# Performance work log

Hardware: AMD Instinct MI355X
Metric: run time of the kernel (lower is better)

Reference implementation:

```python
import jax, jax.numpy as jnp
import numpy as np

B, N, D, S = 16, 128, 128, 128   # batch, n_nodes, node/edge feat dim, state_dim
MP_INT = 256
UP_INT = 256
EPS = 1e-3  # keras BatchNormalization default epsilon


def _mlp(x, W1, b1, W2, b2):
    # Dense(relu) -> Dense(relu)
    h = jax.nn.relu(x @ W1 + b1)
    return jax.nn.relu(h @ W2 + b2)


def setup_inputs() -> dict:
    key = jax.random.key(0)
    ks = jax.random.split(key, 16)
    g = lambda k, shape: jax.random.normal(k, shape, dtype=jnp.float32) * 0.05
    nodes = jax.random.normal(ks[0], (B, N, D), dtype=jnp.float32)
    edges = jax.random.normal(ks[1], (B, N * N, D), dtype=jnp.float32)
    mask = (jax.random.uniform(ks[2], (B, N * N, 1)) > 0.5).astype(jnp.float32)
    return {
        "nodes": nodes, "edges": edges, "mask": mask,
        # Adj_Updater_1: concat(node_i, node_j, edge_ij) -> UP_INT -> S
        "W1a": g(ks[3], (3 * D, UP_INT)), "b1a": jnp.zeros((UP_INT,), jnp.float32),
        "W2a": g(ks[4], (UP_INT, S)), "b2a": jnp.zeros((S,), jnp.float32),
        # Message_Passer_1: concat(node_i, node_j, new_edge) -> MP_INT -> S
        "W1m": g(ks[5], (2 * D + S, MP_INT)), "b1m": jnp.zeros((MP_INT,), jnp.float32),
        "W2m": g(ks[6], (MP_INT, S)), "b2m": jnp.zeros((S,), jnp.float32),
        # Update_Func_1: concat(old_state, agg_messages) -> UP_INT -> S
        "W1u": g(ks[7], (D + S, UP_INT)), "b1u": jnp.zeros((UP_INT,), jnp.float32),
        "W2u": g(ks[8], (UP_INT, S)), "b2u": jnp.zeros((S,), jnp.float32),
        # BatchNorm (inference mode: moving stats) for nodes and edges
        "gamma_n": jnp.ones((S,), jnp.float32), "beta_n": jnp.zeros((S,), jnp.float32),
        "mean_n": jnp.zeros((S,), jnp.float32), "var_n": jnp.ones((S,), jnp.float32),
        "gamma_e": jnp.ones((S,), jnp.float32), "beta_e": jnp.zeros((S,), jnp.float32),
        "mean_e": jnp.zeros((S,), jnp.float32), "var_e": jnp.ones((S,), jnp.float32),
    }


def reference(nodes, edges, mask,
              W1a, b1a, W2a, b2a,
              W1m, b1m, W2m, b2m,
              W1u, b1u, W2u, b2u,
              gamma_n, beta_n, mean_n, var_n,
              gamma_e, beta_e, mean_e, var_e):
    b, n, d = nodes.shape
    # tf.tile(nodes,[1,n,1]): row p*n+q -> nodes[q]  (state_i)
    state_i = jnp.broadcast_to(nodes[:, None, :, :], (b, n, n, d)).reshape(b, n * n, d)
    # reshape(tile(nodes,[1,1,n])): row p*n+q -> nodes[p]  (state_j)
    state_j = jnp.broadcast_to(nodes[:, :, None, :], (b, n, n, d)).reshape(b, n * n, d)

    new_edges = _mlp(jnp.concatenate([state_i, state_j, edges], axis=-1), W1a, b1a, W2a, b2a)
    new_edges = new_edges * mask

    messages = _mlp(jnp.concatenate([state_i, state_j, new_edges], axis=-1), W1m, b1m, W2m, b2m)
    masked = (messages * mask).reshape(b, n, n, -1)
    agg_m = masked.sum(axis=2)  # reduce over axis 2 as in Message_Agg

    state_1 = _mlp(jnp.concatenate([nodes, agg_m], axis=-1), W1u, b1u, W2u, b2u)

    bn = lambda x, g_, b_, m_, v_: g_ * (x - m_) * jax.lax.rsqrt(v_ + EPS) + b_
    nodes_out = bn(state_1, gamma_n, beta_n, mean_n, var_n)
    edges_out = bn(new_edges, gamma_e, beta_e, mean_e, var_e)
    return nodes_out, edges_out
```

## Files before the change

### kernel.cpp

```cpp
#include <hip/hip_runtime.h>
#include <hip/hip_bf16.h>
#include <cstdint>
#include <cstddef>


typedef __attribute__((ext_vector_type(8))) __bf16 bf16x8;
typedef __attribute__((ext_vector_type(4))) float f32x4;

#define GLDS(gp, lp)                                                        \
  __builtin_amdgcn_global_load_lds(                                         \
      (const __attribute__((address_space(1))) void*)(gp),                  \
      (__attribute__((address_space(3))) void*)(lp), 16, 0, 0)

__device__ inline bf16x8 load8_cvt(const float* __restrict__ p) {
  const float4 a = *(const float4*)p;
  const float4 b = *(const float4*)(p + 4);
  bf16x8 r;
  r[0] = (__bf16)a.x; r[1] = (__bf16)a.y; r[2] = (__bf16)a.z; r[3] = (__bf16)a.w;
  r[4] = (__bf16)b.x; r[5] = (__bf16)b.y; r[6] = (__bf16)b.z; r[7] = (__bf16)b.w;
  return r;
}

__global__ void __launch_bounds__(256) proj_kernel(
    const float* __restrict__ nodes, const float* __restrict__ W1a,
    const float* __restrict__ b1a, const float* __restrict__ W1m,
    const float* __restrict__ b1m, const float* __restrict__ ge,
    const float* __restrict__ be, const float* __restrict__ me,
    const float* __restrict__ ve, float* __restrict__ outP,
    float* __restrict__ agg) {
  __shared__ float x[8][128];
  const int mat = blockIdx.y;
  const int t = threadIdx.x;
  if (mat == 0) {
#pragma unroll
    for (int i = 0; i < 4; ++i) agg[blockIdx.x * 1024 + i * 256 + t] = 0.f;
  }
  const float* W = (mat < 2 ? W1a : W1m) + ((mat & 1) ? 128 * 256 : 0);
  float* out = outP + (size_t)mat * (2048 * 256);
  const int r0 = blockIdx.x * 8;
  for (int i = t; i < 1024; i += 256)
    x[i >> 7][i & 127] = nodes[r0 * 128 + i];
  __syncthreads();
  float bv = 0.f;
  if (mat == 1) bv = b1a[t];
  if (mat == 3) {
    bv = b1m[t];
    const float* We = W1m + 65536;
    float cc = 0.f;
    for (int k = 0; k < 128; ++k) {
      float sc = ge[k] * rsqrtf(ve[k] + 1e-3f);
      float sh = be[k] - me[k] * sc;
      cc -= (sh / sc) * We[k * 256 + t];
    }
    bv += cc;
  }
  float acc[8];
#pragma unroll
  for (int r = 0; r < 8; ++r) acc[r] = bv;
  for (int k = 0; k < 128; ++k) {
    float w = W[k * 256 + t];
#pragma unroll
    for (int r = 0; r < 8; ++r) acc[r] += x[r][k] * w;
  }
  if (mat == 0 || mat == 2) {
    const int bb = r0 >> 7, q0 = r0 & 127;
    float* o = out + ((size_t)((bb << 8) + t) << 7) + q0;
#pragma unroll
    for (int r = 0; r < 8; ++r) o[r] = acc[r];
  } else {
    for (int r = 0; r < 8; ++r) out[(size_t)(r0 + r) * 256 + t] = acc[r];
  }
}

__global__ void __launch_bounds__(256) wswz_kernel(
    const float* __restrict__ W1a, const float* __restrict__ W2a,
    const float* __restrict__ W1m, const float* __restrict__ W2m,
    const float* __restrict__ ge, const float* __restrict__ ve,
    __hip_bfloat16* __restrict__ dstp) {
  __bf16* dst = (__bf16*)dstp;
  const int mat = blockIdx.y;
  const float* src;
  __bf16* d;
  int nsh;
  if (mat == 0)      { src = W1a + 65536; d = dst;         nsh = 8; }
  else if (mat == 1) { src = W2a;         d = dst + 32768; nsh = 7; }
  else if (mat == 2) { src = W1m + 65536; d = dst + 65536; nsh = 8; }
  else               { src = W2m;         d = dst + 98304; nsh = 7; }
  const int nmask = (1 << nsh) - 1;
  const int base = (blockIdx.x * 256 + threadIdx.x) * 4;
#pragma unroll
  for (int i = 0; i < 4; ++i) {
    int s = base + i;
    int k = s >> nsh, n = s & nmask;
    float v = src[s];
    if (mat == 2) v *= sqrtf(ve[k] + 1e-3f) / ge[k];
    int g = k >> 3;
    if (nsh == 8) {
      int gs = (g & 8) | ((g ^ n) & 7);
      d[n * 128 + gs * 8 + (k & 7)] = (__bf16)v;
    } else {
      int gs = (g ^ n) & 7;
      d[((k >> 6) << 13) + (n << 6) + (gs << 3) + (k & 7)] = (__bf16)v;
    }
  }
}

__global__ void __launch_bounds__(512, 2) edge_mlp_kernel(
    const float* __restrict__ edges, const float* __restrict__ mask,
    const float* __restrict__ b2a, const float* __restrict__ ge,
    const float* __restrict__ be, const float* __restrict__ me,
    const float* __restrict__ ve, const float* __restrict__ PaT,
    const float* __restrict__ Qab, const __hip_bfloat16* __restrict__ Wsw,
    float* __restrict__ edges_out) {
  __shared__ __align__(16) char sW[131072];
  __shared__ __align__(16) char sH1[16384];

  const int t = threadIdx.x;
  const int lane = t & 63, wv = t >> 6;
  const int cl = lane & 15, qd = lane >> 4;
  const int m0 = wv << 4;

  {
    const char* g = (const char*)Wsw;
    for (int o = wv * 1024; o < 131072; o += 8192)
      GLDS(g + o + lane * 16, sW + o);
  }
  float b2v[8], scv[8], shv[8];
#pragma unroll
  for (int nt = 0; nt < 8; ++nt) {
    const int col = nt * 16 + cl;
    b2v[nt] = b2a[col];
    float sc = ge[col] * rsqrtf(ve[col] + 1e-3f);
    scv[nt] = sc;
    shv[nt] = be[col] - me[col] * sc;
  }
  __syncthreads();

  const int tile0 = blockIdx.x * 8;
  const int bb = tile0 >> 7;

  bf16x8 xfA[4];
  {
    const float* Xb = edges + ((size_t)tile0 << 14);
#pragma unroll
    for (int ks = 0; ks < 4; ++ks)
      xfA[ks] = load8_cvt(Xb + (m0 + cl) * 128 + ks * 32 + qd * 8);
  }

#pragma unroll 1
  for (int ti = 0; ti < 8; ++ti) {
    const int p = (tile0 + ti) & 127;
    bf16x8 xfN[4];
    {
      const float* Xb = edges + ((size_t)(tile0 + ((ti + 1) & 7)) << 14);
#pragma unroll
      for (int ks = 0; ks < 4; ++ks)
        xfN[ks] = load8_cvt(Xb + (m0 + cl) * 128 + ks * 32 + qd * 8);
    }
    const float4 mv =
        *(const float4*)&mask[(bb << 14) + (p << 7) + m0 + qd * 4];
    const float* Qr = Qab + ((size_t)((bb << 7) + p) << 8);

    f32x4 ne[8];
#pragma unroll
    for (int nt = 0; nt < 8; ++nt)
      ne[nt] = (f32x4){b2v[nt], b2v[nt], b2v[nt], b2v[nt]};

#pragma unroll
    for (int h = 0; h < 4; ++h) {
      f32x4 a1[4];
#pragma unroll
      for (int nt = 0; nt < 4; ++nt) {
        const int col = h * 64 + nt * 16 + cl;
        const float qv = Qr[col];
        const float4 pa =
            *(const float4*)&PaT[((size_t)((bb << 8) + col) << 7) + m0 + qd * 4];
        a1[nt] = (f32x4){pa.x + qv, pa.y + qv, pa.z + qv, pa.w + qv};
      }
#pragma unroll
      for (int ks = 0; ks < 4; ++ks)
#pragma unroll
        for (int nt = 0; nt < 4; ++nt) {
          const int nl = nt * 16 + cl;
          const int g = ks * 4 + qd;
          const int gs = (g & 8) | ((g ^ nl) & 7);
          bf16x8 bw = *(const bf16x8*)(sW + (h * 64 + nl) * 256 + gs * 16);
          a1[nt] = __builtin_amdgcn_mfma_f32_16x16x32_bf16(xfA[ks], bw, a1[nt], 0, 0, 0);
        }
#pragma unroll
      for (int nt = 0; nt < 4; ++nt) {
        const int kq = nt * 16 + cl;
#pragma unroll
        for (int r = 0; r < 4; ++r) {
          const int m = m0 + qd * 4 + r;
          float v = a1[nt][r];
          v = v > 0.f ? v : 0.f;
          *(__bf16*)(sH1 + m * 128 + ((((kq >> 3) ^ m) & 7) << 4) +
                     ((kq & 7) << 1)) = (__bf16)v;
        }
      }
      bf16x8 hf[2];
#pragma unroll
      for (int ks = 0; ks < 2; ++ks) {
        const int m = m0 + cl;
        const int gs = ((ks * 4 + qd) ^ m) & 7;
        hf[ks] = *(const bf16x8*)(sH1 + m * 128 + gs * 16);
      }
#pragma unroll
      for (int ks = 0; ks < 2; ++ks)
#pragma unroll
        for (int nt = 0; nt < 8; ++nt) {
          const int n = nt * 16 + cl;
          const int gs = ((ks * 4 + qd) ^ n) & 7;
          bf16x8 bw =
              *(const bf16x8*)(sW + 65536 + h * 16384 + n * 128 + gs * 16);
          ne[nt] = __builtin_amdgcn_mfma_f32_16x16x32_bf16(hf[ks], bw, ne[nt], 0, 0, 0);
        }
    }
    float* Ob = edges_out + ((size_t)(tile0 + ti) << 14);
#pragma unroll
    for (int nt = 0; nt < 8; ++nt) {
      const int col = nt * 16 + cl;
#pragma unroll
      for (int r = 0; r < 4; ++r) {
        const int m = m0 + qd * 4 + r;
        float v = ne[nt][r];
        v = v > 0.f ? v : 0.f;
        const float mr = (r == 0 ? mv.x : r == 1 ? mv.y : r == 2 ? mv.z : mv.w);
        Ob[m * 128 + col] = (v * mr) * scv[nt] + shv[nt];
      }
    }
#pragma unroll
    for (int i = 0; i < 4; ++i) xfA[i] = xfN[i];
  }
}

__global__ void __launch_bounds__(512, 2) msg_mlp_kernel(
    const float* __restrict__ Yedges, const float* __restrict__ mask,
    const float* __restrict__ b2m, const float* __restrict__ PmT,
    const float* __restrict__ Qmb, const __hip_bfloat16* __restrict__ Wsw,
    float* __restrict__ agg) {
  __shared__ __align__(16) char sW[131072];
  __shared__ __align__(16) char sH1[16384];

  const int t = threadIdx.x;
  const int lane = t & 63, wv = t >> 6;
  const int cl = lane & 15, qd = lane >> 4;
  const int m0 = wv << 4;

  {
    const char* g = (const char*)Wsw;
    for (int o = wv * 1024; o < 131072; o += 8192)
      GLDS(g + o + lane * 16, sW + o);
  }
  float b2v[8];
#pragma unroll
  for (int nt = 0; nt < 8; ++nt) b2v[nt] = b2m[nt * 16 + cl];
  __syncthreads();

  const int tile0 = blockIdx.x * 8;
  const int bb = tile0 >> 7;

  bf16x8 xfA[4];
  {
    const float* Xb = Yedges + ((size_t)tile0 << 14);
#pragma unroll
    for (int ks = 0; ks < 4; ++ks)
      xfA[ks] = load8_cvt(Xb + (m0 + cl) * 128 + ks * 32 + qd * 8);
  }

#pragma unroll 1
  for (int ti = 0; ti < 8; ++ti) {
    const int p = (tile0 + ti) & 127;
    bf16x8 xfN[4];
    {
      const float* Xb = Yedges + ((size_t)(tile0 + ((ti + 1) & 7)) << 14);
#pragma unroll
      for (int ks = 0; ks < 4; ++ks)
        xfN[ks] = load8_cvt(Xb + (m0 + cl) * 128 + ks * 32 + qd * 8);
    }
    const float4 mv =
        *(const float4*)&mask[(bb << 14) + (p << 7) + m0 + qd * 4];
    const float* Qr = Qmb + ((size_t)((bb << 7) + p) << 8);

    f32x4 ms[8];
#pragma unroll
    for (int nt = 0; nt < 8; ++nt)
      ms[nt] = (f32x4){b2v[nt], b2v[nt], b2v[nt], b2v[nt]};

#pragma unroll
    for (int h = 0; h < 4; ++h) {
      f32x4 a1[4];
#pragma unroll
      for (int nt = 0; nt < 4; ++nt) {
        const int col = h * 64 + nt * 16 + cl;
        const float qv = Qr[col];
        const float4 pa =
            *(const float4*)&PmT[((size_t)((bb << 8) + col) << 7) + m0 + qd * 4];
        a1[nt] = (f32x4){pa.x + qv, pa.y + qv, pa.z + qv, pa.w + qv};
      }
#pragma unroll
      for (int ks = 0; ks < 4; ++ks)
#pragma unroll
        for (int nt = 0; nt < 4; ++nt) {
          const int nl = nt * 16 + cl;
          const int g = ks * 4 + qd;
          const int gs = (g & 8) | ((g ^ nl) & 7);
          bf16x8 bw = *(const bf16x8*)(sW + (h * 64 + nl) * 256 + gs * 16);
          a1[nt] = __builtin_amdgcn_mfma_f32_16x16x32_bf16(xfA[ks], bw, a1[nt], 0, 0, 0);
        }
#pragma unroll
      for (int nt = 0; nt < 4; ++nt) {
        const int kq = nt * 16 + cl;
#pragma unroll
        for (int r = 0; r < 4; ++r) {
          const int m = m0 + qd * 4 + r;
          float v = a1[nt][r];
          v = v > 0.f ? v : 0.f;
          *(__bf16*)(sH1 + m * 128 + ((((kq >> 3) ^ m) & 7) << 4) +
                     ((kq & 7) << 1)) = (__bf16)v;
        }
      }
      bf16x8 hf[2];
#pragma unroll
      for (int ks = 0; ks < 2; ++ks) {
        const int m = m0 + cl;
        const int gs = ((ks * 4 + qd) ^ m) & 7;
        hf[ks] = *(const bf16x8*)(sH1 + m * 128 + gs * 16);
      }
#pragma unroll
      for (int ks = 0; ks < 2; ++ks)
#pragma unroll
        for (int nt = 0; nt < 8; ++nt) {
          const int n = nt * 16 + cl;
          const int gs = ((ks * 4 + qd) ^ n) & 7;
          bf16x8 bw =
              *(const bf16x8*)(sW + 65536 + h * 16384 + n * 128 + gs * 16);
          ms[nt] = __builtin_amdgcn_mfma_f32_16x16x32_bf16(hf[ks], bw, ms[nt], 0, 0, 0);
        }
    }
#pragma unroll
    for (int nt = 0; nt < 8; ++nt) {
      float s = 0.f;
#pragma unroll
      for (int r = 0; r < 4; ++r) {
        float v = ms[nt][r];
        v = v > 0.f ? v : 0.f;
        const float mr = (r == 0 ? mv.x : r == 1 ? mv.y : r == 2 ? mv.z : mv.w);
        s += v * mr;
      }
      s += __shfl_xor(s, 16);
      s += __shfl_xor(s, 32);
      if (lane < 16)
        atomicAdd(&agg[((size_t)((bb << 7) + p) << 7) + nt * 16 + lane], s);
    }
#pragma unroll
    for (int i = 0; i < 4; ++i) xfA[i] = xfN[i];
  }
}

__global__ void __launch_bounds__(256) update_kernel(
    const float* __restrict__ nodes, const float* __restrict__ agg,
    const float* __restrict__ W1u, const float* __restrict__ b1u,
    const float* __restrict__ W2u, const float* __restrict__ b2u,
    const float* __restrict__ gn, const float* __restrict__ btn,
    const float* __restrict__ mn, const float* __restrict__ vn,
    float* __restrict__ out) {
  __shared__ float x[8][256];
  __shared__ float hh[8][256];
  const int t = threadIdx.x;
  const int r0 = blockIdx.x * 8;
  for (int i = t; i < 2048; i += 256) {
    int r = i >> 8, c = i & 255;
    x[r][c] = (c < 128) ? nodes[(r0 + r) * 128 + c] : agg[(r0 + r) * 128 + (c - 128)];
  }
  __syncthreads();
  float acc[8];
  {
    float bv = b1u[t];
#pragma unroll
    for (int r = 0; r < 8; ++r) acc[r] = bv;
  }
  for (int k = 0; k < 256; ++k) {
    float w = W1u[k * 256 + t];
#pragma unroll
    for (int r = 0; r < 8; ++r) acc[r] += x[r][k] * w;
  }
#pragma unroll
  for (int r = 0; r < 8; ++r) hh[r][t] = acc[r] > 0.f ? acc[r] : 0.f;
  __syncthreads();
  const int j = t & 127, half = t >> 7;
  float a2[4];
  {
    float bv = b2u[j];
#pragma unroll
    for (int r = 0; r < 4; ++r) a2[r] = bv;
  }
  for (int k = 0; k < 256; ++k) {
    float w = W2u[k * 128 + j];
#pragma unroll
    for (int r = 0; r < 4; ++r) a2[r] += hh[half * 4 + r][k] * w;
  }
  float sc = gn[j] * rsqrtf(vn[j] + 1e-3f);
  float sh = btn[j] - mn[j] * sc;
#pragma unroll
  for (int r = 0; r < 4; ++r) {
    float v = a2[r] > 0.f ? a2[r] : 0.f;
    out[(r0 + half * 4 + r) * 128 + j] = v * sc + sh;
  }
}

extern "C" void kernel_launch(void* const* d_in, const int* in_sizes, int n_in,
                              void* d_out, int out_size, void* d_ws,
                              size_t ws_size, hipStream_t stream) {
  (void)in_sizes; (void)n_in; (void)out_size; (void)ws_size;
  const float* nodes = (const float*)d_in[0];
  const float* edges = (const float*)d_in[1];
  const float* mask = (const float*)d_in[2];
  const float* W1a = (const float*)d_in[3];
  const float* b1a = (const float*)d_in[4];
  const float* W2a = (const float*)d_in[5];
  const float* b2a = (const float*)d_in[6];
  const float* W1m = (const float*)d_in[7];
  const float* b1m = (const float*)d_in[8];
  const float* W2m = (const float*)d_in[9];
  const float* b2m = (const float*)d_in[10];
  const float* W1u = (const float*)d_in[11];
  const float* b1u = (const float*)d_in[12];
  const float* W2u = (const float*)d_in[13];
  const float* b2u = (const float*)d_in[14];
  const float* gn = (const float*)d_in[15];
  const float* btn = (const float*)d_in[16];
  const float* mn = (const float*)d_in[17];
  const float* vn = (const float*)d_in[18];
  const float* ge = (const float*)d_in[19];
  const float* be = (const float*)d_in[20];
  const float* me = (const float*)d_in[21];
  const float* ve = (const float*)d_in[22];

  float* out_nodes = (float*)d_out;
  float* out_edges = (float*)d_out + 262144;

  char* ws = (char*)d_ws;
  float* PaT = (float*)(ws);
  float* Qab = (float*)(ws + ((size_t)1 << 21));
  float* PmT = (float*)(ws + ((size_t)2 << 21));
  float* Qmb = (float*)(ws + ((size_t)3 << 21));
  float* agg = (float*)(ws + ((size_t)4 << 21));
  __hip_bfloat16* Wsw = (__hip_bfloat16*)(ws + ((size_t)4 << 21) + ((size_t)1 << 20));

  proj_kernel<<<dim3(256, 4), 256, 0, stream>>>(nodes, W1a, b1a, W1m, b1m, ge,
                                                be, me, ve, PaT, agg);
  wswz_kernel<<<dim3(32, 4), 256, 0, stream>>>(W1a, W2a, W1m, W2m, ge, ve, Wsw);
  edge_mlp_kernel<<<256, 512, 0, stream>>>(edges, mask, b2a, ge, be, me, ve,
                                           PaT, Qab, Wsw, out_edges);
  msg_mlp_kernel<<<256, 512, 0, stream>>>(out_edges, mask, b2m, PmT, Qmb,
                                          Wsw + 65536, agg);
  update_kernel<<<256, 256, 0, stream>>>(nodes, agg, W1u, b1u, W2u, b2u, gn, btn,
                                         mn, vn, out_nodes);
}
```

Before: 524.4 us.

## Give each wave two 16-row M tiles and process two p-tiles per pass

In the edge and message MLP kernels, each wave now computes two 16-row M subtiles. Each B fragment read from shared memory therefore feeds two MFMAs, which halves LDS weight traffic per output. The 8 waves are split into two groups that handle two different p tiles at once, so each block runs 4 passes instead of 8. Each wave gets a private H1 scratch area in shared memory. Block indices are also swizzled to change which blocks run at the same time, and the next tile's input prefetch moves to after the first layer-1 chunk. The cost is more accumulator registers per wave (2x8 f32x4 plus 2x4 for layer 1), which may cause spills or lower occupancy under launch_bounds(512,2).

```diff
diff --git a/kernel.cpp b/kernel.cpp
--- a/kernel.cpp
+++ b/kernel.cpp
@@ -118,7 +118,9 @@
   const int t = threadIdx.x;
   const int lane = t & 63, wv = t >> 6;
   const int cl = lane & 15, qd = lane >> 4;
-  const int m0 = wv << 4;
+  const int tsel = wv >> 2;
+  const int wrow = (wv & 3) * 32;
+  char* const sH1w = sH1 + wv * 2048;
 
   {
     const char* g = (const char*)Wsw;
@@ -136,47 +138,56 @@
   }
   __syncthreads();
 
-  const int tile0 = blockIdx.x * 8;
-  const int bb = tile0 >> 7;
-
-  bf16x8 xfA[4];
+  const int bid = blockIdx.x;
+  const int sw = ((bid & 7) << 5) + (bid >> 3);
+  const int bb = sw >> 4;
+  const int pbase = (sw & 15) * 8;
+  const float* PaTb = PaT + ((size_t)bb << 15);
+
+  bf16x8 xf[2][4], xfN[2][4];
   {
-    const float* Xb = edges + ((size_t)tile0 << 14);
-#pragma unroll
-    for (int ks = 0; ks < 4; ++ks)
-      xfA[ks] = load8_cvt(Xb + (m0 + cl) * 128 + ks * 32 + qd * 8);
+    const float* Xb = edges + ((size_t)((bb << 7) + pbase + tsel) << 14);
+#pragma unroll
+    for (int mt = 0; mt < 2; ++mt)
+#pragma unroll
+      for (int ks = 0; ks < 4; ++ks)
+        xf[mt][ks] = load8_cvt(Xb + (wrow + mt * 16 + cl) * 128 + ks * 32 + qd * 8);
   }
 
 #pragma unroll 1
-  for (int ti = 0; ti < 8; ++ti) {
-    const int p = (tile0 + ti) & 127;
-    bf16x8 xfN[4];
-    {
-      const float* Xb = edges + ((size_t)(tile0 + ((ti + 1) & 7)) << 14);
-#pragma unroll
-      for (int ks = 0; ks < 4; ++ks)
-        xfN[ks] = load8_cvt(Xb + (m0 + cl) * 128 + ks * 32 + qd * 8);
-    }
-    const float4 mv =
-        *(const float4*)&mask[(bb << 14) + (p << 7) + m0 + qd * 4];
+  for (int pass = 0; pass < 4; ++pass) {
+    const int p = pbase + pass * 2 + tsel;
     const float* Qr = Qab + ((size_t)((bb << 7) + p) << 8);
-
-    f32x4 ne[8];
-#pragma unroll
-    for (int nt = 0; nt < 8; ++nt)
-      ne[nt] = (f32x4){b2v[nt], b2v[nt], b2v[nt], b2v[nt]};
+    float qv[4][4];
+#pragma unroll
+    for (int h = 0; h < 4; ++h)
+#pragma unroll
+      for (int nt = 0; nt < 4; ++nt) qv[h][nt] = Qr[h * 64 + nt * 16 + cl];
+    float4 mv[2];
+#pragma unroll
+    for (int mt = 0; mt < 2; ++mt)
+      mv[mt] = *(const float4*)&mask[(bb << 14) + (p << 7) + wrow + mt * 16 + qd * 4];
+
+    f32x4 ne[2][8];
+#pragma unroll
+    for (int mt = 0; mt < 2; ++mt)
+#pragma unroll
+      for (int nt = 0; nt < 8; ++nt)
+        ne[mt][nt] = (f32x4){b2v[nt], b2v[nt], b2v[nt], b2v[nt]};
 
 #pragma unroll
     for (int h = 0; h < 4; ++h) {
-      f32x4 a1[4];
-#pragma unroll
-      for (int nt = 0; nt < 4; ++nt) {
-        const int col = h * 64 + nt * 16 + cl;
-        const float qv = Qr[col];
-        const float4 pa =
-            *(const float4*)&PaT[((size_t)((bb << 8) + col) << 7) + m0 + qd * 4];
-        a1[nt] = (f32x4){pa.x + qv, pa.y + qv, pa.z + qv, pa.w + qv};
-      }
+      f32x4 a1[2][4];
+#pragma unroll
+      for (int mt = 0; mt < 2; ++mt)
+#pragma unroll
+        for (int nt = 0; nt < 4; ++nt) {
+          const int col = h * 64 + nt * 16 + cl;
+          const float4 pa =
+              *(const float4*)&PaTb[((size_t)col << 7) + wrow + mt * 16 + qd * 4];
+          const float q = qv[h][nt];
+          a1[mt][nt] = (f32x4){pa.x + q, pa.y + q, pa.z + q, pa.w + q};
+        }
 #pragma unroll
       for (int ks = 0; ks < 4; ++ks)
 #pragma unroll
@@ -185,26 +196,38 @@
           const int g = ks * 4 + qd;
           const int gs = (g & 8) | ((g ^ nl) & 7);
           bf16x8 bw = *(const bf16x8*)(sW + (h * 64 + nl) * 256 + gs * 16);
-          a1[nt] = __builtin_amdgcn_mfma_f32_16x16x32_bf16(xfA[ks], bw, a1[nt], 0, 0, 0);
-        }
-#pragma unroll
-      for (int nt = 0; nt < 4; ++nt) {
-        const int kq = nt * 16 + cl;
-#pragma unroll
-        for (int r = 0; r < 4; ++r) {
-          const int m = m0 + qd * 4 + r;
-          float v = a1[nt][r];
-          v = v > 0.f ? v : 0.f;
-          *(__bf16*)(sH1 + m * 128 + ((((kq >> 3) ^ m) & 7) << 4) +
-                     ((kq & 7) << 1)) = (__bf16)v;
-        }
+          a1[0][nt] = __builtin_amdgcn_mfma_f32_16x16x32_bf16(xf[0][ks], bw, a1[0][nt], 0, 0, 0);
+          a1[1][nt] = __builtin_amdgcn_mfma_f32_16x16x32_bf16(xf[1][ks], bw, a1[1][nt], 0, 0, 0);
+        }
+      if (h == 0 && pass < 3) {
+        const float* Xb = edges + ((size_t)((bb << 7) + p + 2) << 14);
+#pragma unroll
+        for (int mt = 0; mt < 2; ++mt)
+#pragma unroll
+          for (int ks = 0; ks < 4; ++ks)
+            xfN[mt][ks] =
+                load8_cvt(Xb + (wrow + mt * 16 + cl) * 128 + ks * 32 + qd * 8);
       }
-      bf16x8 hf[2];
-#pragma unroll
-      for (int ks = 0; ks < 2; ++ks) {
-        const int m = m0 + cl;
-        const int gs = ((ks * 4 + qd) ^ m) & 7;
-        hf[ks] = *(const bf16x8*)(sH1 + m * 128 + gs * 16);
+      bf16x8 hf[2][2];
+#pragma unroll
+      for (int mt = 0; mt < 2; ++mt) {
+#pragma unroll
+        for (int nt = 0; nt < 4; ++nt) {
+          const int kq = nt * 16 + cl;
+#pragma unroll
+          for (int r = 0; r < 4; ++r) {
+            const int m = qd * 4 + r;
+            float v = a1[mt][nt][r];
+            v = v > 0.f ? v : 0.f;
+            *(__bf16*)(sH1w + m * 128 + ((((kq >> 3) ^ m) & 7) << 4) +
+                       ((kq & 7) << 1)) = (__bf16)v;
+          }
+        }
+#pragma unroll
+        for (int ks = 0; ks < 2; ++ks) {
+          const int gs = ((ks * 4 + qd) ^ cl) & 7;
+          hf[mt][ks] = *(const bf16x8*)(sH1w + cl * 128 + gs * 16);
+        }
       }
 #pragma unroll
       for (int ks = 0; ks < 2; ++ks)
@@ -214,24 +237,32 @@
           const int gs = ((ks * 4 + qd) ^ n) & 7;
           bf16x8 bw =
               *(const bf16x8*)(sW + 65536 + h * 16384 + n * 128 + gs * 16);
-          ne[nt] = __builtin_amdgcn_mfma_f32_16x16x32_bf16(hf[ks], bw, ne[nt], 0, 0, 0);
-        }
-    }
-    float* Ob = edges_out + ((size_t)(tile0 + ti) << 14);
-#pragma unroll
-    for (int nt = 0; nt < 8; ++nt) {
-      const int col = nt * 16 + cl;
-#pragma unroll
-      for (int r = 0; r < 4; ++r) {
-        const int m = m0 + qd * 4 + r;
-        float v = ne[nt][r];
-        v = v > 0.f ? v : 0.f;
-        const float mr = (r == 0 ? mv.x : r == 1 ? mv.y : r == 2 ? mv.z : mv.w);
-        Ob[m * 128 + col] = (v * mr) * scv[nt] + shv[nt];
+          ne[0][nt] = __builtin_amdgcn_mfma_f32_16x16x32_bf16(hf[0][ks], bw, ne[0][nt], 0, 0, 0);
+          ne[1][nt] = __builtin_amdgcn_mfma_f32_16x16x32_bf16(hf[1][ks], bw, ne[1][nt], 0, 0, 0);
+        }
+    }
+    float* Ob = edges_out + ((size_t)((bb << 7) + p) << 14);
+#pragma unroll
+    for (int mt = 0; mt < 2; ++mt)
+#pragma unroll
+      for (int nt = 0; nt < 8; ++nt) {
+        const int col = nt * 16 + cl;
+#pragma unroll
+        for (int r = 0; r < 4; ++r) {
+          const int m = wrow + mt * 16 + qd * 4 + r;
+          float v = ne[mt][nt][r];
+          v = v > 0.f ? v : 0.f;
+          const float mr =
+              (r == 0 ? mv[mt].x : r == 1 ? mv[mt].y : r == 2 ? mv[mt].z : mv[mt].w);
+          Ob[m * 128 + col] = (v * mr) * scv[nt] + shv[nt];
+        }
       }
-    }
-#pragma unroll
-    for (int i = 0; i < 4; ++i) xfA[i] = xfN[i];
+    if (pass < 3) {
+#pragma unroll
+      for (int mt = 0; mt < 2; ++mt)
+#pragma unroll
+        for (int ks = 0; ks < 4; ++ks) xf[mt][ks] = xfN[mt][ks];
+    }
   }
 }
 
@@ -246,7 +277,9 @@
   const int t = threadIdx.x;
   const int lane = t & 63, wv = t >> 6;
   const int cl = lane & 15, qd = lane >> 4;
-  const int m0 = wv << 4;
+  const int tsel = wv >> 2;
+  const int wrow = (wv & 3) * 32;
+  char* const sH1w = sH1 + wv * 2048;
 
   {
     const char* g = (const char*)Wsw;
@@ -258,47 +291,56 @@
   for (int nt = 0; nt < 8; ++nt) b2v[nt] = b2m[nt * 16 + cl];
   __syncthreads();
 
-  const int tile0 = blockIdx.x * 8;
-  const int bb = tile0 >> 7;
-
-  bf16x8 xfA[4];
+  const int bid = blockIdx.x;
+  const int sw = ((bid & 7) << 5) + (bid >> 3);
+  const int bb = sw >> 4;
+  const int pbase = (sw & 15) * 8;
+  const float* PmTb = PmT + ((size_t)bb << 15);
+
+  bf16x8 xf[2][4], xfN[2][4];
   {
-    const float* Xb = Yedges + ((size_t)tile0 << 14);
-#pragma unroll
-    for (int ks = 0; ks < 4; ++ks)
-      xfA[ks] = load8_cvt(Xb + (m0 + cl) * 128 + ks * 32 + qd * 8);
+    const float* Xb = Yedges + ((size_t)((bb << 7) + pbase + tsel) << 14);
+#pragma unroll
+    for (int mt = 0; mt < 2; ++mt)
+#pragma unroll
+      for (int ks = 0; ks < 4; ++ks)
+        xf[mt][ks] = load8_cvt(Xb + (wrow + mt * 16 + cl) * 128 + ks * 32 + qd * 8);
   }
 
 #pragma unroll 1
-  for (int ti = 0; ti < 8; ++ti) {
-    const int p = (tile0 + ti) & 127;
-    bf16x8 xfN[4];
-    {
-      const float* Xb = Yedges + ((size_t)(tile0 + ((ti + 1) & 7)) << 14);
-#pragma unroll
-      for (int ks = 0; ks < 4; ++ks)
-        xfN[ks] = load8_cvt(Xb + (m0 + cl) * 128 + ks * 32 + qd * 8);
-    }
-    const float4 mv =
-        *(const float4*)&mask[(bb << 14) + (p << 7) + m0 + qd * 4];
+  for (int pass = 0; pass < 4; ++pass) {
+    const int p = pbase + pass * 2 + tsel;
     const float* Qr = Qmb + ((size_t)((bb << 7) + p) << 8);
-
-    f32x4 ms[8];
-#pragma unroll
-    for (int nt = 0; nt < 8; ++nt)
-      ms[nt] = (f32x4){b2v[nt], b2v[nt], b2v[nt], b2v[nt]};
+    float qv[4][4];
+#pragma unroll
+    for (int h = 0; h < 4; ++h)
+#pragma unroll
+      for (int nt = 0; nt < 4; ++nt) qv[h][nt] = Qr[h * 64 + nt * 16 + cl];
+    float4 mv[2];
+#pragma unroll
+    for (int mt = 0; mt < 2; ++mt)
+      mv[mt] = *(const float4*)&mask[(bb << 14) + (p << 7) + wrow + mt * 16 + qd * 4];
+
+    f32x4 ms[2][8];
+#pragma unroll
+    for (int mt = 0; mt < 2; ++mt)
+#pragma unroll
+      for (int nt = 0; nt < 8; ++nt)
+        ms[mt][nt] = (f32x4){b2v[nt], b2v[nt], b2v[nt], b2v[nt]};
 
 #pragma unroll
     for (int h = 0; h < 4; ++h) {
-      f32x4 a1[4];
-#pragma unroll
-      for (int nt = 0; nt < 4; ++nt) {
-        const int col = h * 64 + nt * 16 + cl;
-        const float qv = Qr[col];
-        const float4 pa =
-            *(const float4*)&PmT[((size_t)((bb << 8) + col) << 7) + m0 + qd * 4];
-        a1[nt] = (f32x4){pa.x + qv, pa.y + qv, pa.z + qv, pa.w + qv};
-      }
+      f32x4 a1[2][4];
+#pragma unroll
+      for (int mt = 0; mt < 2; ++mt)
+#pragma unroll
+        for (int nt = 0; nt < 4; ++nt) {
+          const int col = h * 64 + nt * 16 + cl;
+          const float4 pa =
+              *(const float4*)&PmTb[((size_t)col << 7) + wrow + mt * 16 + qd * 4];
+          const float q = qv[h][nt];
+          a1[mt][nt] = (f32x4){pa.x + q, pa.y + q, pa.z + q, pa.w + q};
+        }
 #pragma unroll
       for (int ks = 0; ks < 4; ++ks)
 #pragma unroll
@@ -307,26 +349,38 @@
           const int g = ks * 4 + qd;
           const int gs = (g & 8) | ((g ^ nl) & 7);
           bf16x8 bw = *(const bf16x8*)(sW + (h * 64 + nl) * 256 + gs * 16);
-          a1[nt] = __builtin_amdgcn_mfma_f32_16x16x32_bf16(xfA[ks], bw, a1[nt], 0, 0, 0);
-        }
-#pragma unroll
-      for (int nt = 0; nt < 4; ++nt) {
-        const int kq = nt * 16 + cl;
-#pragma unroll
-        for (int r = 0; r < 4; ++r) {
-          const int m = m0 + qd * 4 + r;
-          float v = a1[nt][r];
-          v = v > 0.f ? v : 0.f;
-          *(__bf16*)(sH1 + m * 128 + ((((kq >> 3) ^ m) & 7) << 4) +
-                     ((kq & 7) << 1)) = (__bf16)v;
-        }
+          a1[0][nt] = __builtin_amdgcn_mfma_f32_16x16x32_bf16(xf[0][ks], bw, a1[0][nt], 0, 0, 0);
+          a1[1][nt] = __builtin_amdgcn_mfma_f32_16x16x32_bf16(xf[1][ks], bw, a1[1][nt], 0, 0, 0);
+        }
+      if (h == 0 && pass < 3) {
+        const float* Xb = Yedges + ((size_t)((bb << 7) + p + 2) << 14);
+#pragma unroll
+        for (int mt = 0; mt < 2; ++mt)
+#pragma unroll
+          for (int ks = 0; ks < 4; ++ks)
+            xfN[mt][ks] =
+                load8_cvt(Xb + (wrow + mt * 16 + cl) * 128 + ks * 32 + qd * 8);
       }
-      bf16x8 hf[2];
-#pragma unroll
-      for (int ks = 0; ks < 2; ++ks) {
-        const int m = m0 + cl;
-        const int gs = ((ks * 4 + qd) ^ m) & 7;
-        hf[ks] = *(const bf16x8*)(sH1 + m * 128 + gs * 16);
+      bf16x8 hf[2][2];
+#pragma unroll
+      for (int mt = 0; mt < 2; ++mt) {
+#pragma unroll
+        for (int nt = 0; nt < 4; ++nt) {
+          const int kq = nt * 16 + cl;
+#pragma unroll
+          for (int r = 0; r < 4; ++r) {
+            const int m = qd * 4 + r;
+            float v = a1[mt][nt][r];
+            v = v > 0.f ? v : 0.f;
+            *(__bf16*)(sH1w + m * 128 + ((((kq >> 3) ^ m) & 7) << 4) +
+                       ((kq & 7) << 1)) = (__bf16)v;
+          }
+        }
+#pragma unroll
+        for (int ks = 0; ks < 2; ++ks) {
+          const int gs = ((ks * 4 + qd) ^ cl) & 7;
+          hf[mt][ks] = *(const bf16x8*)(sH1w + cl * 128 + gs * 16);
+        }
       }
 #pragma unroll
       for (int ks = 0; ks < 2; ++ks)
@@ -336,26 +390,34 @@
           const int gs = ((ks * 4 + qd) ^ n) & 7;
           bf16x8 bw =
               *(const bf16x8*)(sW + 65536 + h * 16384 + n * 128 + gs * 16);
-          ms[nt] = __builtin_amdgcn_mfma_f32_16x16x32_bf16(hf[ks], bw, ms[nt], 0, 0, 0);
+          ms[0][nt] = __builtin_amdgcn_mfma_f32_16x16x32_bf16(hf[0][ks], bw, ms[0][nt], 0, 0, 0);
+          ms[1][nt] = __builtin_amdgcn_mfma_f32_16x16x32_bf16(hf[1][ks], bw, ms[1][nt], 0, 0, 0);
         }
     }
 #pragma unroll
     for (int nt = 0; nt < 8; ++nt) {
       float s = 0.f;
 #pragma unroll
-      for (int r = 0; r < 4; ++r) {
-        float v = ms[nt][r];
-        v = v > 0.f ? v : 0.f;
-        const float mr = (r == 0 ? mv.x : r == 1 ? mv.y : r == 2 ? mv.z : mv.w);
-        s += v * mr;
-      }
+      for (int mt = 0; mt < 2; ++mt)
+#pragma unroll
+        for (int r = 0; r < 4; ++r) {
+          float v = ms[mt][nt][r];
+          v = v > 0.f ? v : 0.f;
+          const float mr =
+              (r == 0 ? mv[mt].x : r == 1 ? mv[mt].y : r == 2 ? mv[mt].z : mv[mt].w);
+          s += v * mr;
+        }
       s += __shfl_xor(s, 16);
       s += __shfl_xor(s, 32);
       if (lane < 16)
         atomicAdd(&agg[((size_t)((bb << 7) + p) << 7) + nt * 16 + lane], s);
     }
-#pragma unroll
-    for (int i = 0; i < 4; ++i) xfA[i] = xfN[i];
+    if (pass < 3) {
+#pragma unroll
+      for (int mt = 0; mt < 2; ++mt)
+#pragma unroll
+        for (int ks = 0; ks < 4; ++ks) xf[mt][ks] = xfN[mt][ks];
+    }
   }
 }
 
```

Result: slower. 641.7 us (+22.4%).
